# Performance work log

Measured on AMD Instinct MI355X. Metric: run time of the kernel, lower is better.

## Reference

```python
import jax, jax.numpy as jnp
import numpy as np

B, N, LQ, DK, DV, DD = 2, 16, 512, 64, 64, 128
TEMPERATURE = 8.0  # sqrt(DK)
NEG_INF = -1e9


def setup_inputs() -> dict:
    key = jax.random.key(0)
    ks = jax.random.split(key, 9)
    h2 = 2 * DD  # dc hidden width = d0 + d1
    return {
        "q": jax.random.normal(ks[0], (B, N, LQ, DK), jnp.float32),
        "k": jax.random.normal(ks[1], (B, N, LQ, DK), jnp.float32),
        "v": jax.random.normal(ks[2], (B, N, LQ, DV), jnp.float32),
        "d0": jax.random.normal(ks[3], (B, LQ, DD), jnp.float32),
        "d1": jax.random.normal(ks[4], (B, LQ, DD), jnp.float32),
        "W1": jax.random.normal(ks[5], (h2, h2), jnp.float32) / np.sqrt(h2),
        "b1": jnp.zeros((h2,), jnp.float32),
        "W2": jax.random.normal(ks[6], (h2, 2), jnp.float32) / np.sqrt(h2),
        "b2": jnp.zeros((2,), jnp.float32),
    }


def reference(q, k, v, d0, d1, W1, b1, W2, b2):
    b, n, lq, dk = q.shape
    dd = d0.shape[-1]
    # pairwise features: f[b,i,j] = concat(d0[b,i], d1[b,j])  -> [b,lq,lq,2dd]
    f = jnp.concatenate(
        [
            jnp.broadcast_to(d0[:, :, None, :], (b, lq, lq, dd)),
            jnp.broadcast_to(d1[:, None, :, :], (b, lq, lq, dd)),
        ],
        axis=-1,
    )
    h = jax.nn.relu(jnp.einsum("bijf,fg->bijg", f, W1) + b1)
    logits = jnp.einsum("bijg,gc->bijc", h, W2) + b2  # [b,lq,lq,2]
    # eval-mode gumbel_softmax(hard=True, tau=1, training=False): argmax of logits
    decisions = (jnp.argmax(logits, axis=-1) == 1)[:, None, :, :]  # [b,1,lq,lq]
    attn = jnp.einsum("bnid,bnjd->bnij", q / TEMPERATURE, k)
    attn = jnp.where(decisions, attn, NEG_INF)
    attn = jax.nn.softmax(attn, axis=-1)  # dropout is identity in eval mode
    output = jnp.einsum("bnij,bnjd->bnid", attn, v)
    return output, attn, decisions
```

## Files before the change

### kernel.cpp

```cpp
#include <hip/hip_runtime.h>

#define BB 2
#define NN 16
#define LQ 512
#define DKk 64
#define DVv 64
#define DDd 128
#define H2 256
#define NEG_INF -1e9f

__global__ __launch_bounds__(256) void mlp_stage1(
    const float* __restrict__ d0, const float* __restrict__ d1,
    const float* __restrict__ W1, const float* __restrict__ b1,
    double* __restrict__ U64, double* __restrict__ W64,
    float* __restrict__ U32, float* __restrict__ W32)
{
    __shared__ float drow[2][DDd];
    int gid = blockIdx.x;
    int half = gid >> 9;
    int r0 = (gid & 511) * 2;
    const float* din = half ? d1 : d0;
    int w1off = half ? DDd : 0;
    double* o64 = half ? W64 : U64;
    float* o32 = half ? W32 : U32;
    int t = threadIdx.x;
    drow[t >> 7][t & 127] = din[(size_t)(r0 + (t >> 7)) * DDd + (t & 127)];
    __syncthreads();
    int g = t;
    double acc[2] = {};
#pragma unroll 2
    for (int f = 0; f < DDd; f += 4) {
        double w0 = (double)W1[(w1off + f + 0) * H2 + g];
        double w1 = (double)W1[(w1off + f + 1) * H2 + g];
        double w2 = (double)W1[(w1off + f + 2) * H2 + g];
        double w3 = (double)W1[(w1off + f + 3) * H2 + g];
#pragma unroll
        for (int r = 0; r < 2; ++r) {
            float4 dr = *(const float4*)&drow[r][f];
            acc[r] = fma((double)dr.x, w0, acc[r]);
            acc[r] = fma((double)dr.y, w1, acc[r]);
            acc[r] = fma((double)dr.z, w2, acc[r]);
            acc[r] = fma((double)dr.w, w3, acc[r]);
        }
    }
    double bb = half ? 0.0 : (double)b1[g];
#pragma unroll
    for (int r = 0; r < 2; ++r) {
        double a = acc[r] + bb;
        o64[(size_t)(r0 + r) * H2 + g] = a;
        o32[(size_t)(r0 + r) * H2 + g] = (float)a;
    }
}

__global__ __launch_bounds__(256, 2) void dec_full(
    const float* __restrict__ U32, const float* __restrict__ W32,
    const double* __restrict__ U64, const double* __restrict__ W64,
    const float* __restrict__ W2, const float* __restrict__ b2,
    float* __restrict__ dec_out)
{
    __shared__ __align__(16) float Ut[H2][36];
    __shared__ __align__(16) float Wt[H2][36];
    __shared__ float gvs[H2];
    __shared__ int lbuf[1024];
    __shared__ int lcnt;
    int bid = blockIdx.x;
    int b  = bid >> 8;
    int i0 = ((bid >> 4) & 15) * 32;
    int j0 = (bid & 15) * 32;
    int t = threadIdx.x;
    gvs[t] = W2[t * 2 + 1] - W2[t * 2];
    if (t == 0) lcnt = 0;
    float bias = b2[1] - b2[0];
    {
        int r = t >> 3, gq = t & 7;
        const float* su = U32 + ((size_t)(b * LQ) + i0 + r) * H2;
        const float* sw = W32 + ((size_t)(b * LQ) + j0 + r) * H2;
#pragma unroll
        for (int s = 0; s < 8; ++s) {
            int g = gq * 4 + s * 32;
            float4 u4 = *(const float4*)(su + g);
            Ut[g + 0][r] = u4.x; Ut[g + 1][r] = u4.y;
            Ut[g + 2][r] = u4.z; Ut[g + 3][r] = u4.w;
            float4 w4 = *(const float4*)(sw + g);
            Wt[g + 0][r] = w4.x; Wt[g + 1][r] = w4.y;
            Wt[g + 2][r] = w4.z; Wt[g + 3][r] = w4.w;
        }
    }
    __syncthreads();
    int pi = t >> 4, pj = t & 15;
    float a00 = 0.f, a01 = 0.f, a10 = 0.f, a11 = 0.f;
#pragma unroll 8
    for (int g = 0; g < H2; ++g) {
        float2 u2 = *(const float2*)&Ut[g][pi * 2];
        float2 w2 = *(const float2*)&Wt[g][pj * 2];
        float gv = gvs[g];
        a00 = fmaf(fmaxf(u2.x + w2.x, 0.f), gv, a00);
        a01 = fmaf(fmaxf(u2.x + w2.y, 0.f), gv, a01);
        a10 = fmaf(fmaxf(u2.y + w2.x, 0.f), gv, a10);
        a11 = fmaf(fmaxf(u2.y + w2.y, 0.f), gv, a11);
    }
    int row0 = b * LQ + i0 + pi * 2;
    float g00 = a00 + bias, g01 = a01 + bias;
    float g10 = a10 + bias, g11 = a11 + bias;
    int jb = j0 + pj * 2;
    *(float2*)&dec_out[(size_t)row0 * LQ + jb] =
        make_float2(g00 > 0.f ? 1.f : 0.f, g01 > 0.f ? 1.f : 0.f);
    *(float2*)&dec_out[(size_t)(row0 + 1) * LQ + jb] =
        make_float2(g10 > 0.f ? 1.f : 0.f, g11 > 0.f ? 1.f : 0.f);
    if (fabsf(g00) < 2e-2f) { int lx = atomicAdd(&lcnt, 1); lbuf[lx] = (row0 << 9) | jb; }
    if (fabsf(g01) < 2e-2f) { int lx = atomicAdd(&lcnt, 1); lbuf[lx] = (row0 << 9) | (jb + 1); }
    if (fabsf(g10) < 2e-2f) { int lx = atomicAdd(&lcnt, 1); lbuf[lx] = ((row0 + 1) << 9) | jb; }
    if (fabsf(g11) < 2e-2f) { int lx = atomicAdd(&lcnt, 1); lbuf[lx] = ((row0 + 1) << 9) | (jb + 1); }
    __syncthreads();
    int nloc = lcnt;
    int wv = t >> 6, ln = t & 63;
    for (int x = wv; x < nloc; x += 4) {
        int pij = lbuf[x];
        int j = pij & (LQ - 1);
        int prow = pij >> 9;
        int pb = prow >> 9;
        const double* u = U64 + (size_t)prow * H2;
        const double* w = W64 + ((size_t)(pb * LQ) + j) * H2;
        double acc = 0.0;
        for (int g = ln; g < H2; g += 64) {
            double tv = u[g] + w[g];
            tv = tv > 0.0 ? tv : 0.0;
            acc = fma(tv, (double)W2[g * 2 + 1] - (double)W2[g * 2 + 0], acc);
        }
#pragma unroll
        for (int off = 32; off; off >>= 1) acc += __shfl_xor(acc, off, 64);
        if (ln == 0) {
            acc += (double)b2[1] - (double)b2[0];
            dec_out[(size_t)prow * LQ + j] = acc > 0.0 ? 1.f : 0.f;
        }
    }
}

__global__ __launch_bounds__(256) void fused_attn(
    const float* __restrict__ q, const float* __restrict__ k,
    const float* __restrict__ v, const float* __restrict__ dec,
    float* __restrict__ attn, float* __restrict__ out)
{
    __shared__ __align__(16) float smem[10752];
    float* qT = smem;
    float* kT = smem + 2304;
    float* Pt = smem;
    float* Vs = smem + 2112;
    int bid = blockIdx.x;
    int bn = bid >> 4;
    int i0 = (bid & 15) * 32;
    int b = bn >> 4;
    int t = threadIdx.x;

    {
        int qi = t >> 3;
        const float* src = q + ((size_t)bn * LQ + i0 + qi) * DKk;
#pragma unroll
        for (int it = 0; it < 2; ++it) {
            int kkq = (t & 7) + it * 8;
            float4 t4 = *(const float4*)(src + kkq * 4);
            qT[(kkq * 4 + 0) * 36 + qi] = t4.x;
            qT[(kkq * 4 + 1) * 36 + qi] = t4.y;
            qT[(kkq * 4 + 2) * 36 + qi] = t4.z;
            qT[(kkq * 4 + 3) * 36 + qi] = t4.w;
        }
    }
    int tiq = t >> 5;
    int tjq = t & 31;
    float s[4][4][4];

#pragma unroll
    for (int c = 0; c < 4; ++c) {
        __syncthreads();
        {
            int kj = t >> 2;
#pragma unroll
            for (int it = 0; it < 8; ++it) {
                int jj = kj + (it & 1) * 64;
                int kkq = (t & 3) + (it >> 1) * 4;
                float4 t4 = *(const float4*)(k + ((size_t)bn * LQ + c * 128 + jj) * DKk + kkq * 4);
                kT[(kkq * 4 + 0) * 132 + jj] = t4.x;
                kT[(kkq * 4 + 1) * 132 + jj] = t4.y;
                kT[(kkq * 4 + 2) * 132 + jj] = t4.z;
                kT[(kkq * 4 + 3) * 132 + jj] = t4.w;
            }
        }
        __syncthreads();
        float acc[4][4] = {};
#pragma unroll 8
        for (int kk = 0; kk < 64; ++kk) {
            float4 a  = *(const float4*)&qT[kk * 36 + tiq * 4];
            float4 bb = *(const float4*)&kT[kk * 132 + tjq * 4];
            acc[0][0] = fmaf(a.x, bb.x, acc[0][0]); acc[0][1] = fmaf(a.x, bb.y, acc[0][1]);
            acc[0][2] = fmaf(a.x, bb.z, acc[0][2]); acc[0][3] = fmaf(a.x, bb.w, acc[0][3]);
            acc[1][0] = fmaf(a.y, bb.x, acc[1][0]); acc[1][1] = fmaf(a.y, bb.y, acc[1][1]);
            acc[1][2] = fmaf(a.y, bb.z, acc[1][2]); acc[1][3] = fmaf(a.y, bb.w, acc[1][3]);
            acc[2][0] = fmaf(a.z, bb.x, acc[2][0]); acc[2][1] = fmaf(a.z, bb.y, acc[2][1]);
            acc[2][2] = fmaf(a.z, bb.z, acc[2][2]); acc[2][3] = fmaf(a.z, bb.w, acc[2][3]);
            acc[3][0] = fmaf(a.w, bb.x, acc[3][0]); acc[3][1] = fmaf(a.w, bb.y, acc[3][1]);
            acc[3][2] = fmaf(a.w, bb.z, acc[3][2]); acc[3][3] = fmaf(a.w, bb.w, acc[3][3]);
        }
#pragma unroll
        for (int r = 0; r < 4; ++r) {
            float4 m4 = *(const float4*)&dec[((size_t)(b * LQ) + i0 + tiq * 4 + r) * LQ + c * 128 + tjq * 4];
            s[c][r][0] = m4.x != 0.f ? acc[r][0] * 0.125f : NEG_INF;
            s[c][r][1] = m4.y != 0.f ? acc[r][1] * 0.125f : NEG_INF;
            s[c][r][2] = m4.z != 0.f ? acc[r][2] * 0.125f : NEG_INF;
            s[c][r][3] = m4.w != 0.f ? acc[r][3] * 0.125f : NEG_INF;
        }
    }
#pragma unroll
    for (int r = 0; r < 4; ++r) {
        float m = NEG_INF;
#pragma unroll
        for (int c = 0; c < 4; ++c)
#pragma unroll
            for (int cc = 0; cc < 4; ++cc) m = fmaxf(m, s[c][r][cc]);
#pragma unroll
        for (int off = 1; off < 32; off <<= 1) m = fmaxf(m, __shfl_xor(m, off, 32));
        float sum = 0.f;
#pragma unroll
        for (int c = 0; c < 4; ++c)
#pragma unroll
            for (int cc = 0; cc < 4; ++cc) {
                float e = __expf(s[c][r][cc] - m);
                s[c][r][cc] = e; sum += e;
            }
#pragma unroll
        for (int off = 1; off < 32; off <<= 1) sum += __shfl_xor(sum, off, 32);
        float inv = 1.f / sum;
#pragma unroll
        for (int c = 0; c < 4; ++c)
#pragma unroll
            for (int cc = 0; cc < 4; ++cc) s[c][r][cc] *= inv;
    }
#pragma unroll
    for (int c = 0; c < 4; ++c)
#pragma unroll
        for (int r = 0; r < 4; ++r) {
            float4 wv = make_float4(s[c][r][0], s[c][r][1], s[c][r][2], s[c][r][3]);
            *(float4*)&attn[((size_t)bn * LQ + i0 + tiq * 4 + r) * LQ + c * 128 + tjq * 4] = wv;
        }

    int jh = t >> 7;
    int ih = (t >> 4) & 7;
    int dh = t & 15;
    float o[4][4] = {};
#pragma unroll
    for (int c8 = 0; c8 < 8; ++c8) {
        __syncthreads();
        if ((tjq >> 4) == (c8 & 1)) {
            int jl4 = tjq & 15;
            int c = c8 >> 1;
#pragma unroll
            for (int cc = 0; cc < 4; ++cc) {
                int row = jl4 * 4 + cc;
                *(float4*)&Pt[row * 32 + ((tiq ^ (row & 7)) << 2)] =
                    make_float4(s[c][0][cc], s[c][1][cc], s[c][2][cc], s[c][3][cc]);
            }
        }
        {
            int vj = t >> 2;
#pragma unroll
            for (int it = 0; it < 4; ++it) {
                int dq = (t & 3) + it * 4;
                *(float4*)&Vs[vj * 68 + dq * 4] =
                    *(const float4*)(v + ((size_t)bn * LQ + c8 * 64 + vj) * DVv + dq * 4);
            }
        }
        __syncthreads();
#pragma unroll 8
        for (int jx = 0; jx < 32; ++jx) {
            int jj = jh * 32 + jx;
            float4 p4 = *(const float4*)&Pt[jj * 32 + ((ih ^ (jj & 7)) << 2)];
            float4 v4 = *(const float4*)&Vs[jj * 68 + dh * 4];
            o[0][0] = fmaf(p4.x, v4.x, o[0][0]); o[0][1] = fmaf(p4.x, v4.y, o[0][1]);
            o[0][2] = fmaf(p4.x, v4.z, o[0][2]); o[0][3] = fmaf(p4.x, v4.w, o[0][3]);
            o[1][0] = fmaf(p4.y, v4.x, o[1][0]); o[1][1] = fmaf(p4.y, v4.y, o[1][1]);
            o[1][2] = fmaf(p4.y, v4.z, o[1][2]); o[1][3] = fmaf(p4.y, v4.w, o[1][3]);
            o[2][0] = fmaf(p4.z, v4.x, o[2][0]); o[2][1] = fmaf(p4.z, v4.y, o[2][1]);
            o[2][2] = fmaf(p4.z, v4.z, o[2][2]); o[2][3] = fmaf(p4.z, v4.w, o[2][3]);
            o[3][0] = fmaf(p4.w, v4.x, o[3][0]); o[3][1] = fmaf(p4.w, v4.y, o[3][1]);
            o[3][2] = fmaf(p4.w, v4.z, o[3][2]); o[3][3] = fmaf(p4.w, v4.w, o[3][3]);
        }
    }
    __syncthreads();
    float* red = smem;
    if (jh == 1) {
        int kidx = (ih * 16 + dh) * 20;
#pragma unroll
        for (int rr = 0; rr < 4; ++rr)
            *(float4*)&red[kidx + rr * 4] =
                make_float4(o[rr][0], o[rr][1], o[rr][2], o[rr][3]);
    }
    __syncthreads();
    if (jh == 0) {
        int kidx = (ih * 16 + dh) * 20;
#pragma unroll
        for (int rr = 0; rr < 4; ++rr) {
            float4 p = *(const float4*)&red[kidx + rr * 4];
            *(float4*)&out[((size_t)bn * LQ + i0 + ih * 4 + rr) * DVv + dh * 4] =
                make_float4(o[rr][0] + p.x, o[rr][1] + p.y,
                            o[rr][2] + p.z, o[rr][3] + p.w);
        }
    }
}

extern "C" void kernel_launch(void* const* d_in, const int* in_sizes, int n_in,
                              void* d_out, int out_size, void* d_ws, size_t ws_size,
                              hipStream_t stream)
{
    const float* q  = (const float*)d_in[0];
    const float* k  = (const float*)d_in[1];
    const float* v  = (const float*)d_in[2];
    const float* d0 = (const float*)d_in[3];
    const float* d1 = (const float*)d_in[4];
    const float* W1 = (const float*)d_in[5];
    const float* b1 = (const float*)d_in[6];
    const float* W2 = (const float*)d_in[7];
    const float* b2 = (const float*)d_in[8];

    float* out  = (float*)d_out;
    float* attn = out + (size_t)BB * NN * LQ * DVv;
    float* dec  = attn + (size_t)BB * NN * LQ * LQ;

    char* scratch = (char*)attn;
    double* U64 = (double*)(scratch);
    double* W64 = (double*)(scratch + (2u << 20));
    float*  U32 = (float*) (scratch + (4u << 20));
    float*  W32 = (float*) (scratch + (5u << 20));

    mlp_stage1<<<1024, 256, 0, stream>>>(d0, d1, W1, b1, U64, W64, U32, W32);
    dec_full<<<512, 256, 0, stream>>>(U32, W32, U64, W64, W2, b2, dec);
    fused_attn<<<512, 256, 0, stream>>>(q, k, v, dec, attn, out);
}
```

Baseline: 160.8 us.

## Retile PV product to 8x4 register tiles with four-way j split and new swizzle

Reshapes the P·V accumulation so each thread computes an 8-row by 4-column output tile over a quarter of the key chunk, rather than 4x4 over half. Each V load from shared memory is now reused across twice as many rows. It also switches the P-tile shared-memory swizzle from XOR to a rotation, to keep the paired float4 reads conflict-free. The cost is more accumulator registers and a longer, serialized four-stage cross-thread reduction that needs extra barriers.

```diff
diff --git a/kernel.cpp b/kernel.cpp
--- a/kernel.cpp
+++ b/kernel.cpp
@@ -242,10 +242,10 @@
             *(float4*)&attn[((size_t)bn * LQ + i0 + tiq * 4 + r) * LQ + c * 128 + tjq * 4] = wv;
         }
 
-    int jh = t >> 7;
-    int ih = (t >> 4) & 7;
-    int dh = t & 15;
-    float o[4][4] = {};
+    int jq  = t >> 6;
+    int ih8 = (t >> 4) & 3;
+    int dh  = t & 15;
+    float o[8][4] = {};
 #pragma unroll
     for (int c8 = 0; c8 < 8; ++c8) {
         __syncthreads();
@@ -255,7 +255,7 @@
 #pragma unroll
             for (int cc = 0; cc < 4; ++cc) {
                 int row = jl4 * 4 + cc;
-                *(float4*)&Pt[row * 32 + ((tiq ^ (row & 7)) << 2)] =
+                *(float4*)&Pt[row * 32 + (((tiq + jl4) & 7) << 2)] =
                     make_float4(s[c][0][cc], s[c][1][cc], s[c][2][cc], s[c][3][cc]);
             }
         }
@@ -269,39 +269,67 @@
             }
         }
         __syncthreads();
-#pragma unroll 8
-        for (int jx = 0; jx < 32; ++jx) {
-            int jj = jh * 32 + jx;
-            float4 p4 = *(const float4*)&Pt[jj * 32 + ((ih ^ (jj & 7)) << 2)];
+#pragma unroll 4
+        for (int jx = 0; jx < 16; ++jx) {
+            int jj = jq * 16 + jx;
+            int js = jj >> 2;
+            float4 pl = *(const float4*)&Pt[jj * 32 + (((ih8 * 2 + js) & 7) << 2)];
+            float4 ph = *(const float4*)&Pt[jj * 32 + (((ih8 * 2 + 1 + js) & 7) << 2)];
             float4 v4 = *(const float4*)&Vs[jj * 68 + dh * 4];
-            o[0][0] = fmaf(p4.x, v4.x, o[0][0]); o[0][1] = fmaf(p4.x, v4.y, o[0][1]);
-            o[0][2] = fmaf(p4.x, v4.z, o[0][2]); o[0][3] = fmaf(p4.x, v4.w, o[0][3]);
-            o[1][0] = fmaf(p4.y, v4.x, o[1][0]); o[1][1] = fmaf(p4.y, v4.y, o[1][1]);
-            o[1][2] = fmaf(p4.y, v4.z, o[1][2]); o[1][3] = fmaf(p4.y, v4.w, o[1][3]);
-            o[2][0] = fmaf(p4.z, v4.x, o[2][0]); o[2][1] = fmaf(p4.z, v4.y, o[2][1]);
-            o[2][2] = fmaf(p4.z, v4.z, o[2][2]); o[2][3] = fmaf(p4.z, v4.w, o[2][3]);
-            o[3][0] = fmaf(p4.w, v4.x, o[3][0]); o[3][1] = fmaf(p4.w, v4.y, o[3][1]);
-            o[3][2] = fmaf(p4.w, v4.z, o[3][2]); o[3][3] = fmaf(p4.w, v4.w, o[3][3]);
-        }
-    }
-    __syncthreads();
+            o[0][0] = fmaf(pl.x, v4.x, o[0][0]); o[0][1] = fmaf(pl.x, v4.y, o[0][1]);
+            o[0][2] = fmaf(pl.x, v4.z, o[0][2]); o[0][3] = fmaf(pl.x, v4.w, o[0][3]);
+            o[1][0] = fmaf(pl.y, v4.x, o[1][0]); o[1][1] = fmaf(pl.y, v4.y, o[1][1]);
+            o[1][2] = fmaf(pl.y, v4.z, o[1][2]); o[1][3] = fmaf(pl.y, v4.w, o[1][3]);
+            o[2][0] = fmaf(pl.z, v4.x, o[2][0]); o[2][1] = fmaf(pl.z, v4.y, o[2][1]);
+            o[2][2] = fmaf(pl.z, v4.z, o[2][2]); o[2][3] = fmaf(pl.z, v4.w, o[2][3]);
+            o[3][0] = fmaf(pl.w, v4.x, o[3][0]); o[3][1] = fmaf(pl.w, v4.y, o[3][1]);
+            o[3][2] = fmaf(pl.w, v4.z, o[3][2]); o[3][3] = fmaf(pl.w, v4.w, o[3][3]);
+            o[4][0] = fmaf(ph.x, v4.x, o[4][0]); o[4][1] = fmaf(ph.x, v4.y, o[4][1]);
+            o[4][2] = fmaf(ph.x, v4.z, o[4][2]); o[4][3] = fmaf(ph.x, v4.w, o[4][3]);
+            o[5][0] = fmaf(ph.y, v4.x, o[5][0]); o[5][1] = fmaf(ph.y, v4.y, o[5][1]);
+            o[5][2] = fmaf(ph.y, v4.z, o[5][2]); o[5][3] = fmaf(ph.y, v4.w, o[5][3]);
+            o[6][0] = fmaf(ph.z, v4.x, o[6][0]); o[6][1] = fmaf(ph.z, v4.y, o[6][1]);
+            o[6][2] = fmaf(ph.z, v4.z, o[6][2]); o[6][3] = fmaf(ph.z, v4.w, o[6][3]);
+            o[7][0] = fmaf(ph.w, v4.x, o[7][0]); o[7][1] = fmaf(ph.w, v4.y, o[7][1]);
+            o[7][2] = fmaf(ph.w, v4.z, o[7][2]); o[7][3] = fmaf(ph.w, v4.w, o[7][3]);
+        }
+    }
     float* red = smem;
-    if (jh == 1) {
-        int kidx = (ih * 16 + dh) * 20;
-#pragma unroll
-        for (int rr = 0; rr < 4; ++rr)
-            *(float4*)&red[kidx + rr * 4] =
+    __syncthreads();
+    if (jq == 3) {
+#pragma unroll
+        for (int rr = 0; rr < 8; ++rr)
+            *(float4*)&red[((ih8 * 8 + rr) * 16 + dh) * 20] =
                 make_float4(o[rr][0], o[rr][1], o[rr][2], o[rr][3]);
     }
     __syncthreads();
-    if (jh == 0) {
-        int kidx = (ih * 16 + dh) * 20;
-#pragma unroll
-        for (int rr = 0; rr < 4; ++rr) {
-            float4 p = *(const float4*)&red[kidx + rr * 4];
-            *(float4*)&out[((size_t)bn * LQ + i0 + ih * 4 + rr) * DVv + dh * 4] =
-                make_float4(o[rr][0] + p.x, o[rr][1] + p.y,
-                            o[rr][2] + p.z, o[rr][3] + p.w);
+    if (jq == 2) {
+#pragma unroll
+        for (int rr = 0; rr < 8; ++rr) {
+            float* p = &red[((ih8 * 8 + rr) * 16 + dh) * 20];
+            float4 x = *(const float4*)p;
+            *(float4*)p = make_float4(x.x + o[rr][0], x.y + o[rr][1],
+                                      x.z + o[rr][2], x.w + o[rr][3]);
+        }
+    }
+    __syncthreads();
+    if (jq == 1) {
+#pragma unroll
+        for (int rr = 0; rr < 8; ++rr) {
+            float* p = &red[((ih8 * 8 + rr) * 16 + dh) * 20];
+            float4 x = *(const float4*)p;
+            *(float4*)p = make_float4(x.x + o[rr][0], x.y + o[rr][1],
+                                      x.z + o[rr][2], x.w + o[rr][3]);
+        }
+    }
+    __syncthreads();
+    if (jq == 0) {
+#pragma unroll
+        for (int rr = 0; rr < 8; ++rr) {
+            float4 x = *(const float4*)&red[((ih8 * 8 + rr) * 16 + dh) * 20];
+            *(float4*)&out[((size_t)bn * LQ + i0 + ih8 * 8 + rr) * DVv + dh * 4] =
+                make_float4(x.x + o[rr][0], x.y + o[rr][1],
+                            x.z + o[rr][2], x.w + o[rr][3]);
         }
     }
 }
```

Measured after the change: 162.4 us. No clear change (+1.0%).
